# Kernel tuning notes

Measured on AMD Instinct MI355X. Metric: run time of the kernel, lower is better.

Reference implementation:

```python
import jax, jax.numpy as jnp
import numpy as np

DIM = 128  # matches init kwarg `dim`; scale = dim ** 0.5


def setup_inputs() -> dict:
    key = jax.random.key(0)
    k1, k2, k3, k4 = jax.random.split(key, 4)
    A = 100000
    K = 1600000  # num edges
    z_msg_all = jax.random.normal(k1, (A, DIM), dtype=jnp.float32)
    recv_query_all = jax.random.normal(k2, (A, DIM), dtype=jnp.float32)
    i_idx = jax.random.randint(k3, (K,), 0, A, dtype=jnp.int64)
    j_idx = jax.random.randint(k4, (K,), 0, A, dtype=jnp.int64)
    return {"z_msg_all": z_msg_all, "recv_query_all": recv_query_all,
            "i_idx": i_idx, "j_idx": j_idx, "A": A}


def reference(z_msg_all, recv_query_all, i_idx, j_idx, A):
    # q_j = z[j], k_i = z[i]; per-edge scores; segmented softmax over recipient j;
    # weighted scatter-add of values k_i into pooled[j]. recv_query_all is unused
    # in the original forward (kept for signature fidelity).
    scale = DIM ** 0.5
    k = z_msg_all[i_idx]                     # (K, D) gather
    q = z_msg_all[j_idx]                     # (K, D) gather
    scores = jnp.sum(q * k, axis=-1) / scale  # (K,)
    # segmented softmax (3-pass: amax, exp, sum)
    max_per = jax.ops.segment_max(scores, j_idx, num_segments=A)  # (A,)
    exp = jnp.exp(scores - max_per[j_idx])                         # (K,)
    denom = jax.ops.segment_sum(exp, j_idx, num_segments=A)        # (A,)
    alpha = exp / (denom[j_idx] + 1e-6)                            # (K,)
    # weighted scatter-add of values into recipients
    pooled = jax.ops.segment_sum(alpha[:, None] * k, j_idx, num_segments=A)  # (A, D)
    return pooled
```

## Files before the change

### kernel.cpp

```cpp
#include <hip/hip_runtime.h>
#include <math.h>


typedef unsigned short us8 __attribute__((ext_vector_type(8)));
typedef float f32x2 __attribute__((ext_vector_type(2)));

#define CAP   8192
#define ABLK  512
#define EPB   2048

__device__ inline unsigned short f2bf(float f) {
    unsigned u = __float_as_uint(f);
    return (unsigned short)((u + 0x7fff + ((u >> 16) & 1)) >> 16);
}
__device__ inline float bfhi(unsigned u) { return __uint_as_float(u & 0xffff0000u); }
__device__ inline float bflo(unsigned u) { return __uint_as_float(u << 16); }

__global__ __launch_bounds__(ABLK) void bin_kernel(
        const int* __restrict__ i_idx, const int* __restrict__ j_idx,
        int* __restrict__ gcount, unsigned* __restrict__ binned,
        int K, int NB) {
    int tid = threadIdx.x;

    __shared__ int lhist[ABLK];
    __shared__ int loff[ABLK + 1];
    __shared__ int lcur[ABLK];
    __shared__ int gbase[ABLK];
    __shared__ unsigned staged_p[EPB];
    __shared__ unsigned short staged_b[EPB];

    lhist[tid] = 0;
    __syncthreads();

    int ebase = blockIdx.x * EPB;
    int myi[4], myj[4], myb[4];
    #pragma unroll
    for (int q = 0; q < 4; ++q) {
        int e = ebase + tid + q * ABLK;
        if (e < K) {
            myj[q] = j_idx[e];
            myi[q] = i_idx[e];
            myb[q] = myj[q] >> 8;
            atomicAdd(&lhist[myb[q]], 1);
        } else {
            myb[q] = -1;
        }
    }
    __syncthreads();
    for (int off = 1; off < ABLK; off <<= 1) {
        int v = (tid >= off) ? lhist[tid - off] : 0;
        __syncthreads();
        lhist[tid] += v;
        __syncthreads();
    }
    loff[tid + 1] = lhist[tid];
    if (tid == 0) loff[0] = 0;
    __syncthreads();
    int cntb = loff[tid + 1] - loff[tid];
    if (tid < NB && cntb > 0)
        gbase[tid] = tid * CAP + atomicAdd(&gcount[tid], cntb);
    lcur[tid] = loff[tid];
    __syncthreads();
    #pragma unroll
    for (int q = 0; q < 4; ++q) {
        if (myb[q] >= 0) {
            int p = atomicAdd(&lcur[myb[q]], 1);
            staged_p[p] = ((unsigned)myi[q] << 8) | ((unsigned)myj[q] & 255u);
            staged_b[p] = (unsigned short)myb[q];
        }
    }
    __syncthreads();
    int totE = loff[ABLK];
    for (int idx = tid; idx < totE; idx += ABLK) {
        int bb = staged_b[idx];
        binned[(size_t)gbase[bb] + (idx - loff[bb])] = staged_p[idx];
    }
}

__global__ __launch_bounds__(1024) void finish_kernel(
        const float* __restrict__ z, us8* __restrict__ z16,
        unsigned* __restrict__ binned, const int* __restrict__ gcount,
        int2* __restrict__ seg, int A, int n16) {
    __shared__ unsigned staged[CAP];
    __shared__ int sorted_loc[CAP];
    __shared__ int hist[256];
    __shared__ int offs[257];
    __shared__ int cur[256];

    int b = blockIdx.x;
    int tid = threadIdx.x;

    {
        const float4* __restrict__ z4 = reinterpret_cast<const float4*>(z);
        int gstride = gridDim.x * 1024;
        for (int t = b * 1024 + tid; t < n16; t += gstride) {
            float4 a = z4[(size_t)2 * t];
            float4 c = z4[(size_t)2 * t + 1];
            us8 o;
            o[0] = f2bf(a.x); o[1] = f2bf(a.y); o[2] = f2bf(a.z); o[3] = f2bf(a.w);
            o[4] = f2bf(c.x); o[5] = f2bf(c.y); o[6] = f2bf(c.z); o[7] = f2bf(c.w);
            z16[t] = o;
        }
    }

    int cnt = gcount[b];
    if (cnt > CAP) cnt = CAP;
    unsigned* __restrict__ src = binned + (size_t)b * CAP;

    if (tid < 256) hist[tid] = 0;
    for (int x = tid; x < cnt; x += 1024) staged[x] = src[x];
    __syncthreads();
    for (int x = tid; x < cnt; x += 1024)
        atomicAdd(&hist[staged[x] & 255u], 1);
    __syncthreads();
    for (int off = 1; off < 256; off <<= 1) {
        int v = 0;
        if (tid < 256 && tid >= off) v = hist[tid - off];
        __syncthreads();
        if (tid < 256 && tid >= off) hist[tid] += v;
        __syncthreads();
    }
    if (tid == 0) offs[0] = 0;
    if (tid < 256) offs[tid + 1] = hist[tid];
    __syncthreads();
    if (tid < 256) cur[tid] = offs[tid];
    __syncthreads();
    for (int x = tid; x < cnt; x += 1024) {
        unsigned pk = staged[x];
        int p = atomicAdd(&cur[pk & 255u], 1);
        sorted_loc[p] = (int)(pk >> 8);
    }
    __syncthreads();
    for (int x = tid; x < cnt; x += 1024) src[x] = (unsigned)sorted_loc[x];
    if (tid < 256) {
        int j = (b << 8) + tid;
        if (j < A)
            seg[j] = make_int2(b * CAP + offs[tid], b * CAP + offs[tid + 1]);
    }
}

__global__ __launch_bounds__(256) void attn_kernel(
        const us8* __restrict__ z16,
        const unsigned* __restrict__ sorted_i, const int2* __restrict__ seg,
        float* __restrict__ out, int A) {
    int w = blockIdx.x * 4 + (threadIdx.x >> 6);
    if (w >= A) return;
    int lane = threadIdx.x & 63;
    int g = lane >> 3;
    int r = lane & 7;

    const uint4* __restrict__ zk = reinterpret_cast<const uint4*>(z16);
    const float scale = 0.08838834764831843f * 1.4426950408889634f;

    uint4 uq0 = zk[(size_t)w * 16 + r];
    uint4 uq1 = zk[(size_t)w * 16 + 8 + r];
    f32x2 q2[8];
    q2[0] = f32x2{bflo(uq0.x), bfhi(uq0.x)} * scale;
    q2[1] = f32x2{bflo(uq0.y), bfhi(uq0.y)} * scale;
    q2[2] = f32x2{bflo(uq0.z), bfhi(uq0.z)} * scale;
    q2[3] = f32x2{bflo(uq0.w), bfhi(uq0.w)} * scale;
    q2[4] = f32x2{bflo(uq1.x), bfhi(uq1.x)} * scale;
    q2[5] = f32x2{bflo(uq1.y), bfhi(uq1.y)} * scale;
    q2[6] = f32x2{bflo(uq1.z), bfhi(uq1.z)} * scale;
    q2[7] = f32x2{bflo(uq1.w), bfhi(uq1.w)} * scale;

    int2 s01 = seg[w];

    float l = 0.0f;
    f32x2 acc[8];
    #pragma unroll
    for (int t = 0; t < 8; ++t) acc[t] = f32x2{0.f, 0.f};

    int p = s01.x + g;
    int i_next = (int)sorted_i[p];
    while (p < s01.y) {
        int i = i_next;
        i_next = (int)sorted_i[p + 8];
        uint4 u0 = zk[(size_t)i * 16 + r];
        uint4 u1 = zk[(size_t)i * 16 + 8 + r];
        f32x2 k2[8];
        k2[0] = f32x2{bflo(u0.x), bfhi(u0.x)};
        k2[1] = f32x2{bflo(u0.y), bfhi(u0.y)};
        k2[2] = f32x2{bflo(u0.z), bfhi(u0.z)};
        k2[3] = f32x2{bflo(u0.w), bfhi(u0.w)};
        k2[4] = f32x2{bflo(u1.x), bfhi(u1.x)};
        k2[5] = f32x2{bflo(u1.y), bfhi(u1.y)};
        k2[6] = f32x2{bflo(u1.z), bfhi(u1.z)};
        k2[7] = f32x2{bflo(u1.w), bfhi(u1.w)};

        f32x2 prod = q2[0] * k2[0];
        #pragma unroll
        for (int t = 1; t < 8; ++t) prod += q2[t] * k2[t];
        float part = prod.x + prod.y;
        part += __shfl_xor(part, 1);
        part += __shfl_xor(part, 2);
        part += __shfl_xor(part, 4);

        float pe = exp2f(part);
        l += pe;
        f32x2 pe2 = {pe, pe};
        #pragma unroll
        for (int t = 0; t < 8; ++t) acc[t] += pe2 * k2[t];
        p += 8;
    }

    l += __shfl_xor(l, 8);
    l += __shfl_xor(l, 16);
    l += __shfl_xor(l, 32);

    {
        bool hi = (g & 4) != 0;
        #pragma unroll
        for (int t = 0; t < 4; ++t) {
            f32x2 send = hi ? acc[t] : acc[t + 4];
            f32x2 recv;
            recv.x = __shfl_xor(send.x, 32);
            recv.y = __shfl_xor(send.y, 32);
            f32x2 keep = hi ? acc[t + 4] : acc[t];
            acc[t] = keep + recv;
        }
        hi = (g & 2) != 0;
        #pragma unroll
        for (int t = 0; t < 2; ++t) {
            f32x2 send = hi ? acc[t] : acc[t + 2];
            f32x2 recv;
            recv.x = __shfl_xor(send.x, 16);
            recv.y = __shfl_xor(send.y, 16);
            f32x2 keep = hi ? acc[t + 2] : acc[t];
            acc[t] = keep + recv;
        }
        hi = (g & 1) != 0;
        {
            f32x2 send = hi ? acc[0] : acc[1];
            f32x2 recv;
            recv.x = __shfl_xor(send.x, 8);
            recv.y = __shfl_xor(send.y, 8);
            f32x2 keep = hi ? acc[1] : acc[0];
            acc[0] = keep + recv;
        }
    }

    float inv = 1.0f / (l + 1e-6f);
    float2 o;
    o.x = acc[0].x * inv;
    o.y = acc[0].y * inv;
    int o_idx = ((g & 4) << 3) + 4 * r + (g & 3);
    reinterpret_cast<float2*>(out)[(size_t)w * 64 + o_idx] = o;
}

extern "C" void kernel_launch(void* const* d_in, const int* in_sizes, int n_in,
                              void* d_out, int out_size, void* d_ws, size_t ws_size,
                              hipStream_t stream) {
    const float* z     = (const float*)d_in[0];
    const int*   i_idx = (const int*)d_in[2];
    const int*   j_idx = (const int*)d_in[3];

    const int D = 128;
    int A = in_sizes[0] / D;
    int K = in_sizes[2];
    int n16 = A * (D / 8);
    int NB = (A + 255) >> 8;

    unsigned short* z16 = (unsigned short*)d_ws;
    unsigned* binned = (unsigned*)(z16 + (size_t)A * 128);
    int2* seg = (int2*)(binned + (size_t)NB * CAP);
    int* gcount = (int*)(seg + A);

    float* out = (float*)d_out;

    hipMemsetAsync(gcount, 0, (size_t)NB * sizeof(int), stream);
    bin_kernel<<<(K + EPB - 1) / EPB, ABLK, 0, stream>>>(i_idx, j_idx,
                                                         gcount, binned, K, NB);
    finish_kernel<<<NB, 1024, 0, stream>>>(z, (us8*)z16, binned, gcount, seg,
                                           A, n16);
    attn_kernel<<<(A + 3) / 4, 256, 0, stream>>>((const us8*)z16, binned,
                                                 seg, out, A);
}
```

Baseline: 120.3 us.

## Switch gathered z to fp16 with fdot2, move conversion into bin kernel

Stores the compact copy of z as fp16 using packed round-toward-zero conversion instead of manual bf16 rounding, and computes the edge scores with fdot2 instructions on the packed halves. The scale is now applied after the dot product. The fp32-to-fp16 conversion moves from finish_kernel into bin_kernel. finish_kernel drops to 512 threads, no longer stages the sorted indices in shared memory and scatters them straight to global memory. attn_kernel gets an occupancy hint of 8 blocks. The fp16 range and precision trade-offs differ from bf16 and could affect accuracy for large inputs.

```diff
diff --git a/kernel.cpp b/kernel.cpp
--- a/kernel.cpp
+++ b/kernel.cpp
@@ -2,25 +2,35 @@
 #include <math.h>
 
 
-typedef unsigned short us8 __attribute__((ext_vector_type(8)));
-typedef float f32x2 __attribute__((ext_vector_type(2)));
+typedef _Float16 h2 __attribute__((ext_vector_type(2)));
 
 #define CAP   8192
 #define ABLK  512
 #define EPB   2048
 
-__device__ inline unsigned short f2bf(float f) {
-    unsigned u = __float_as_uint(f);
-    return (unsigned short)((u + 0x7fff + ((u >> 16) & 1)) >> 16);
-}
-__device__ inline float bfhi(unsigned u) { return __uint_as_float(u & 0xffff0000u); }
-__device__ inline float bflo(unsigned u) { return __uint_as_float(u << 16); }
+__device__ inline h2 as_h2(unsigned u) { return __builtin_bit_cast(h2, u); }
 
 __global__ __launch_bounds__(ABLK) void bin_kernel(
+        const float* __restrict__ z, uint4* __restrict__ z16,
         const int* __restrict__ i_idx, const int* __restrict__ j_idx,
         int* __restrict__ gcount, unsigned* __restrict__ binned,
-        int K, int NB) {
+        int n16, int K, int NB) {
     int tid = threadIdx.x;
+
+    {
+        const float4* __restrict__ z4 = reinterpret_cast<const float4*>(z);
+        int nth = gridDim.x * ABLK;
+        for (int t = blockIdx.x * ABLK + tid; t < n16; t += nth) {
+            float4 a = z4[(size_t)2 * t];
+            float4 c = z4[(size_t)2 * t + 1];
+            uint4 o;
+            o.x = __builtin_bit_cast(unsigned, __builtin_amdgcn_cvt_pkrtz(a.x, a.y));
+            o.y = __builtin_bit_cast(unsigned, __builtin_amdgcn_cvt_pkrtz(a.z, a.w));
+            o.z = __builtin_bit_cast(unsigned, __builtin_amdgcn_cvt_pkrtz(c.x, c.y));
+            o.w = __builtin_bit_cast(unsigned, __builtin_amdgcn_cvt_pkrtz(c.z, c.w));
+            z16[t] = o;
+        }
+    }
 
     __shared__ int lhist[ABLK];
     __shared__ int loff[ABLK + 1];
@@ -77,40 +87,24 @@
     }
 }
 
-__global__ __launch_bounds__(1024) void finish_kernel(
-        const float* __restrict__ z, us8* __restrict__ z16,
+__global__ __launch_bounds__(512) void finish_kernel(
         unsigned* __restrict__ binned, const int* __restrict__ gcount,
-        int2* __restrict__ seg, int A, int n16) {
+        int2* __restrict__ seg, int A) {
     __shared__ unsigned staged[CAP];
-    __shared__ int sorted_loc[CAP];
     __shared__ int hist[256];
     __shared__ int offs[257];
     __shared__ int cur[256];
 
     int b = blockIdx.x;
     int tid = threadIdx.x;
-
-    {
-        const float4* __restrict__ z4 = reinterpret_cast<const float4*>(z);
-        int gstride = gridDim.x * 1024;
-        for (int t = b * 1024 + tid; t < n16; t += gstride) {
-            float4 a = z4[(size_t)2 * t];
-            float4 c = z4[(size_t)2 * t + 1];
-            us8 o;
-            o[0] = f2bf(a.x); o[1] = f2bf(a.y); o[2] = f2bf(a.z); o[3] = f2bf(a.w);
-            o[4] = f2bf(c.x); o[5] = f2bf(c.y); o[6] = f2bf(c.z); o[7] = f2bf(c.w);
-            z16[t] = o;
-        }
-    }
-
     int cnt = gcount[b];
     if (cnt > CAP) cnt = CAP;
     unsigned* __restrict__ src = binned + (size_t)b * CAP;
 
     if (tid < 256) hist[tid] = 0;
-    for (int x = tid; x < cnt; x += 1024) staged[x] = src[x];
-    __syncthreads();
-    for (int x = tid; x < cnt; x += 1024)
+    for (int x = tid; x < cnt; x += 512) staged[x] = src[x];
+    __syncthreads();
+    for (int x = tid; x < cnt; x += 512)
         atomicAdd(&hist[staged[x] & 255u], 1);
     __syncthreads();
     for (int off = 1; off < 256; off <<= 1) {
@@ -125,13 +119,11 @@
     __syncthreads();
     if (tid < 256) cur[tid] = offs[tid];
     __syncthreads();
-    for (int x = tid; x < cnt; x += 1024) {
+    for (int x = tid; x < cnt; x += 512) {
         unsigned pk = staged[x];
         int p = atomicAdd(&cur[pk & 255u], 1);
-        sorted_loc[p] = (int)(pk >> 8);
-    }
-    __syncthreads();
-    for (int x = tid; x < cnt; x += 1024) src[x] = (unsigned)sorted_loc[x];
+        src[p] = pk >> 8;
+    }
     if (tid < 256) {
         int j = (b << 8) + tid;
         if (j < A)
@@ -139,8 +131,8 @@
     }
 }
 
-__global__ __launch_bounds__(256) void attn_kernel(
-        const us8* __restrict__ z16,
+__global__ __launch_bounds__(256, 8) void attn_kernel(
+        const uint4* __restrict__ zk,
         const unsigned* __restrict__ sorted_i, const int2* __restrict__ seg,
         float* __restrict__ out, int A) {
     int w = blockIdx.x * 4 + (threadIdx.x >> 6);
@@ -149,27 +141,22 @@
     int g = lane >> 3;
     int r = lane & 7;
 
-    const uint4* __restrict__ zk = reinterpret_cast<const uint4*>(z16);
-    const float scale = 0.08838834764831843f * 1.4426950408889634f;
+    const float kscale = 0.08838834764831843f * 1.4426950408889634f;
 
     uint4 uq0 = zk[(size_t)w * 16 + r];
     uint4 uq1 = zk[(size_t)w * 16 + 8 + r];
-    f32x2 q2[8];
-    q2[0] = f32x2{bflo(uq0.x), bfhi(uq0.x)} * scale;
-    q2[1] = f32x2{bflo(uq0.y), bfhi(uq0.y)} * scale;
-    q2[2] = f32x2{bflo(uq0.z), bfhi(uq0.z)} * scale;
-    q2[3] = f32x2{bflo(uq0.w), bfhi(uq0.w)} * scale;
-    q2[4] = f32x2{bflo(uq1.x), bfhi(uq1.x)} * scale;
-    q2[5] = f32x2{bflo(uq1.y), bfhi(uq1.y)} * scale;
-    q2[6] = f32x2{bflo(uq1.z), bfhi(uq1.z)} * scale;
-    q2[7] = f32x2{bflo(uq1.w), bfhi(uq1.w)} * scale;
+    h2 qh[8];
+    qh[0] = as_h2(uq0.x); qh[1] = as_h2(uq0.y);
+    qh[2] = as_h2(uq0.z); qh[3] = as_h2(uq0.w);
+    qh[4] = as_h2(uq1.x); qh[5] = as_h2(uq1.y);
+    qh[6] = as_h2(uq1.z); qh[7] = as_h2(uq1.w);
 
     int2 s01 = seg[w];
 
     float l = 0.0f;
-    f32x2 acc[8];
+    float acc[16];
     #pragma unroll
-    for (int t = 0; t < 8; ++t) acc[t] = f32x2{0.f, 0.f};
+    for (int d = 0; d < 16; ++d) acc[d] = 0.0f;
 
     int p = s01.x + g;
     int i_next = (int)sorted_i[p];
@@ -178,29 +165,32 @@
         i_next = (int)sorted_i[p + 8];
         uint4 u0 = zk[(size_t)i * 16 + r];
         uint4 u1 = zk[(size_t)i * 16 + 8 + r];
-        f32x2 k2[8];
-        k2[0] = f32x2{bflo(u0.x), bfhi(u0.x)};
-        k2[1] = f32x2{bflo(u0.y), bfhi(u0.y)};
-        k2[2] = f32x2{bflo(u0.z), bfhi(u0.z)};
-        k2[3] = f32x2{bflo(u0.w), bfhi(u0.w)};
-        k2[4] = f32x2{bflo(u1.x), bfhi(u1.x)};
-        k2[5] = f32x2{bflo(u1.y), bfhi(u1.y)};
-        k2[6] = f32x2{bflo(u1.z), bfhi(u1.z)};
-        k2[7] = f32x2{bflo(u1.w), bfhi(u1.w)};
-
-        f32x2 prod = q2[0] * k2[0];
-        #pragma unroll
-        for (int t = 1; t < 8; ++t) prod += q2[t] * k2[t];
-        float part = prod.x + prod.y;
+        h2 kh[8];
+        kh[0] = as_h2(u0.x); kh[1] = as_h2(u0.y);
+        kh[2] = as_h2(u0.z); kh[3] = as_h2(u0.w);
+        kh[4] = as_h2(u1.x); kh[5] = as_h2(u1.y);
+        kh[6] = as_h2(u1.z); kh[7] = as_h2(u1.w);
+
+        float pa = __builtin_amdgcn_fdot2(qh[0], kh[0], 0.0f, false);
+        float pb = __builtin_amdgcn_fdot2(qh[4], kh[4], 0.0f, false);
+        pa = __builtin_amdgcn_fdot2(qh[1], kh[1], pa, false);
+        pb = __builtin_amdgcn_fdot2(qh[5], kh[5], pb, false);
+        pa = __builtin_amdgcn_fdot2(qh[2], kh[2], pa, false);
+        pb = __builtin_amdgcn_fdot2(qh[6], kh[6], pb, false);
+        pa = __builtin_amdgcn_fdot2(qh[3], kh[3], pa, false);
+        pb = __builtin_amdgcn_fdot2(qh[7], kh[7], pb, false);
+        float part = pa + pb;
         part += __shfl_xor(part, 1);
         part += __shfl_xor(part, 2);
         part += __shfl_xor(part, 4);
 
-        float pe = exp2f(part);
+        float pe = exp2f(part * kscale);
         l += pe;
-        f32x2 pe2 = {pe, pe};
         #pragma unroll
-        for (int t = 0; t < 8; ++t) acc[t] += pe2 * k2[t];
+        for (int t = 0; t < 8; ++t) {
+            acc[2 * t]     = fmaf(pe, (float)kh[t].x, acc[2 * t]);
+            acc[2 * t + 1] = fmaf(pe, (float)kh[t].y, acc[2 * t + 1]);
+        }
         p += 8;
     }
 
@@ -212,38 +202,44 @@
         bool hi = (g & 4) != 0;
         #pragma unroll
         for (int t = 0; t < 4; ++t) {
-            f32x2 send = hi ? acc[t] : acc[t + 4];
-            f32x2 recv;
-            recv.x = __shfl_xor(send.x, 32);
-            recv.y = __shfl_xor(send.y, 32);
-            f32x2 keep = hi ? acc[t + 4] : acc[t];
-            acc[t] = keep + recv;
+            float sx = hi ? acc[2 * t]     : acc[2 * t + 8];
+            float sy = hi ? acc[2 * t + 1] : acc[2 * t + 9];
+            float rx = __shfl_xor(sx, 32);
+            float ry = __shfl_xor(sy, 32);
+            float kx = hi ? acc[2 * t + 8] : acc[2 * t];
+            float ky = hi ? acc[2 * t + 9] : acc[2 * t + 1];
+            acc[2 * t]     = kx + rx;
+            acc[2 * t + 1] = ky + ry;
         }
         hi = (g & 2) != 0;
         #pragma unroll
         for (int t = 0; t < 2; ++t) {
-            f32x2 send = hi ? acc[t] : acc[t + 2];
-            f32x2 recv;
-            recv.x = __shfl_xor(send.x, 16);
-            recv.y = __shfl_xor(send.y, 16);
-            f32x2 keep = hi ? acc[t + 2] : acc[t];
-            acc[t] = keep + recv;
+            float sx = hi ? acc[2 * t]     : acc[2 * t + 4];
+            float sy = hi ? acc[2 * t + 1] : acc[2 * t + 5];
+            float rx = __shfl_xor(sx, 16);
+            float ry = __shfl_xor(sy, 16);
+            float kx = hi ? acc[2 * t + 4] : acc[2 * t];
+            float ky = hi ? acc[2 * t + 5] : acc[2 * t + 1];
+            acc[2 * t]     = kx + rx;
+            acc[2 * t + 1] = ky + ry;
         }
         hi = (g & 1) != 0;
         {
-            f32x2 send = hi ? acc[0] : acc[1];
-            f32x2 recv;
-            recv.x = __shfl_xor(send.x, 8);
-            recv.y = __shfl_xor(send.y, 8);
-            f32x2 keep = hi ? acc[1] : acc[0];
-            acc[0] = keep + recv;
+            float sx = hi ? acc[0] : acc[2];
+            float sy = hi ? acc[1] : acc[3];
+            float rx = __shfl_xor(sx, 8);
+            float ry = __shfl_xor(sy, 8);
+            float kx = hi ? acc[2] : acc[0];
+            float ky = hi ? acc[3] : acc[1];
+            acc[0] = kx + rx;
+            acc[1] = ky + ry;
         }
     }
 
     float inv = 1.0f / (l + 1e-6f);
     float2 o;
-    o.x = acc[0].x * inv;
-    o.y = acc[0].y * inv;
+    o.x = acc[0] * inv;
+    o.y = acc[1] * inv;
     int o_idx = ((g & 4) << 3) + 4 * r + (g & 3);
     reinterpret_cast<float2*>(out)[(size_t)w * 64 + o_idx] = o;
 }
@@ -268,11 +264,10 @@
 
     float* out = (float*)d_out;
 
-    hipMemsetAsync(gcount, 0, (size_t)NB * sizeof(int), stream);
-    bin_kernel<<<(K + EPB - 1) / EPB, ABLK, 0, stream>>>(i_idx, j_idx,
-                                                         gcount, binned, K, NB);
-    finish_kernel<<<NB, 1024, 0, stream>>>(z, (us8*)z16, binned, gcount, seg,
-                                           A, n16);
-    attn_kernel<<<(A + 3) / 4, 256, 0, stream>>>((const us8*)z16, binned,
+    (void)hipMemsetAsync(gcount, 0, (size_t)NB * sizeof(int), stream);
+    bin_kernel<<<(K + EPB - 1) / EPB, ABLK, 0, stream>>>(
+        z, (uint4*)z16, i_idx, j_idx, gcount, binned, n16, K, NB);
+    finish_kernel<<<NB, 512, 0, stream>>>(binned, gcount, seg, A);
+    attn_kernel<<<(A + 3) / 4, 256, 0, stream>>>((const uint4*)z16, binned,
                                                  seg, out, A);
 }
```

Result: no change. 119.7 us (-0.5%).
